# Optimization experiments

Measured on AMD Instinct MI355X. Metric: run time of the kernel, lower is better.

The kernel has to match this reference:

```python
import jax, jax.numpy as jnp
import numpy as np

TEMPERATURE = 0.1
EPS = 1e-8

# MatchingRuleAllViews defaults:
#   intra_view_same_class=1, intra_view_different_class=0,
#   inter_view_same_class=1, inter_view_different_class=0,
#   inter_image_same_class=-1, inter_image_different_class=-1,
#   self_similarity=-1

def setup_inputs() -> dict:
    key = jax.random.key(0)
    k1, k2, k3 = jax.random.split(key, 3)
    B, V, C, HW = 2, 2, 64, 1024
    student = jax.random.normal(k1, (B, V, C, HW), dtype=jnp.float32)
    teacher = jax.random.normal(k2, (B, V, C, HW), dtype=jnp.float32)
    labels = jax.random.randint(k3, (B, V, HW), 0, 5, dtype=jnp.int32)
    return {"student_embeddings": student, "teacher_embeddings": teacher, "labels": labels}


def _masks(B, V, HW, labels_flat):
    # image / view / pixel ids for each of the N = B*V*HW flattened positions
    image_ids = jnp.repeat(jnp.arange(B), V * HW)          # [N]
    view_ids = jnp.tile(jnp.repeat(jnp.arange(V), HW), B)  # [N]
    pixel_ids = jnp.tile(jnp.arange(HW), B * V)            # [N]
    si = image_ids[:, None] == image_ids[None, :]
    sv = view_ids[:, None] == view_ids[None, :]
    sp = pixel_ids[:, None] == pixel_ids[None, :]
    sc = labels_flat[:, None] == labels_flat[None, :]
    # default rule: same image -> (same class ? 1 : 0); different image -> -1;
    # self-similarity (same image, view, pixel) -> -1
    mask = jnp.where(si, jnp.where(sc, 1, 0), -1)
    mask = jnp.where(si & sv & sp, -1, mask)
    numerator_mask = (mask == 1).astype(jnp.float32)
    denom_mask = (mask >= 0).astype(jnp.float32)
    return numerator_mask, denom_mask


def reference(student_embeddings, teacher_embeddings, labels):
    B, V, C, HW = student_embeddings.shape
    N = B * V * HW
    # [B,V,C,HW] -> [N,C], L2-normalized
    sf = student_embeddings.transpose(0, 1, 3, 2).reshape(N, C)
    tf = teacher_embeddings.transpose(0, 1, 3, 2).reshape(N, C)
    sf = sf / jnp.linalg.norm(sf, axis=1, keepdims=True).clip(1e-12)
    tf = tf / jnp.linalg.norm(tf, axis=1, keepdims=True).clip(1e-12)
    logits = (sf @ tf.T) / TEMPERATURE  # [N,N]

    labels_flat = labels.reshape(-1)
    numerator_mask, denom_mask = _masks(B, V, HW, labels_flat)

    # masked log-softmax over dim 1 (denominator restricted to denom_mask)
    masked_logits = jnp.where(denom_mask > 0, logits, -jnp.inf)
    log_prob = jax.nn.log_softmax(masked_logits, axis=1)
    log_prob = jnp.where(jnp.isneginf(log_prob), 0.0, log_prob)

    numerator_sums = numerator_mask.sum(1)
    mean_log_prob_pos = (numerator_mask * log_prob).sum(1) / (numerator_sums + EPS)
    valid = numerator_sums > EPS  # [N] bool
    n_valid = valid.sum().astype(jnp.float32)
    loss = -jnp.sum(jnp.where(valid, mean_log_prob_pos, 0.0)) / n_valid

    # bg_anchors=False branch: (loss * non_bg[valid]).sum() / (non_bg[valid].sum() + eps)
    non_bg = (labels_flat != 0).astype(jnp.float32)
    non_bg_valid_sum = jnp.sum(non_bg * valid.astype(jnp.float32))
    loss = (loss * non_bg_valid_sum) / (non_bg_valid_sum + EPS)
    return loss
```

## Files before the change

### kernel.cpp

```cpp
#include <hip/hip_runtime.h>
#include <math.h>

#define NEG_INF (-1e30f)

typedef __attribute__((ext_vector_type(8))) short s16x8;
typedef __attribute__((ext_vector_type(4))) float f32x4;

__device__ __forceinline__ unsigned int pack_bf16(float lo, float hi) {
    unsigned int ul = __float_as_uint(lo);
    ul += 0x7FFFu + ((ul >> 16) & 1u);
    unsigned int uh = __float_as_uint(hi);
    uh += 0x7FFFu + ((uh >> 16) & 1u);
    return (ul >> 16) | (uh & 0xFFFF0000u);
}

__global__ __launch_bounds__(256, 2) void fused_scl_kernel(
    const float* __restrict__ s, const float* __restrict__ t,
    const int* __restrict__ labels, float4* __restrict__ stats,
    float* __restrict__ accums) {

    const int rb = blockIdx.x >> 4;
    const int jc = blockIdx.x & 15;
    const int img = rb >> 4;
    const int i0 = rb * 128;
    const int jb = img * 2048 + jc * 128;

    const int tid = threadIdx.x;

    __shared__ __align__(16) short lds_a[128 * 72];
    __shared__ __align__(16) short lds_b[128 * 72];
    __shared__ float lds_rs[128], lds_rt[128];
    __shared__ int lds_labi[128], lds_labj[128];

    if (blockIdx.x == 0 && tid < 8) accums[tid] = 0.f;

    if (tid < 128) lds_labi[tid] = labels[i0 + tid];
    else           lds_labj[tid - 128] = labels[jb + tid - 128];

    {
        const int t7 = tid & 7;
        const int pos4 = (tid >> 3) << 2;
        const int bvi = ((i0 >> 10) << 16) + (i0 & 1023) + pos4;
        const int bvj = ((jb >> 10) << 16) + (jb & 1023) + pos4;
        unsigned int* wa = (unsigned int*)lds_a;
        unsigned int* wb = (unsigned int*)lds_b;
#pragma unroll
        for (int k = 0; k < 4; ++k) {
            const int c0 = 2 * t7 + 16 * k;
            float4 a0 = *(const float4*)(s + bvi + c0 * 1024);
            float4 a1 = *(const float4*)(s + bvi + (c0 + 1) * 1024);
            float4 b0 = *(const float4*)(t + bvj + c0 * 1024);
            float4 b1 = *(const float4*)(t + bvj + (c0 + 1) * 1024);
            const int w = t7 + 8 * k;
            wa[36 * (pos4 + 0) + w] = pack_bf16(a0.x, a1.x);
            wa[36 * (pos4 + 1) + w] = pack_bf16(a0.y, a1.y);
            wa[36 * (pos4 + 2) + w] = pack_bf16(a0.z, a1.z);
            wa[36 * (pos4 + 3) + w] = pack_bf16(a0.w, a1.w);
            wb[36 * (pos4 + 0) + w] = pack_bf16(b0.x, b1.x);
            wb[36 * (pos4 + 1) + w] = pack_bf16(b0.y, b1.y);
            wb[36 * (pos4 + 2) + w] = pack_bf16(b0.z, b1.z);
            wb[36 * (pos4 + 3) + w] = pack_bf16(b0.w, b1.w);
        }
    }
    __syncthreads();

    {
        const int row = tid & 127;
        const unsigned int* wr =
            (const unsigned int*)((tid < 128) ? lds_a : lds_b) + 36 * row;
        float ssq = 0.f;
#pragma unroll
        for (int i = 0; i < 8; ++i) {
            uint4 u4 = *(const uint4*)(wr + 4 * i);
            const unsigned int uu[4] = {u4.x, u4.y, u4.z, u4.w};
#pragma unroll
            for (int q = 0; q < 4; ++q) {
                float lo = __uint_as_float(uu[q] << 16);
                float hi = __uint_as_float(uu[q] & 0xFFFF0000u);
                ssq = fmaf(lo, lo, ssq);
                ssq = fmaf(hi, hi, ssq);
            }
        }
        float r = 1.f / fmaxf(sqrtf(ssq), 1e-12f);
        if (tid < 128) lds_rs[row] = r;
        else           lds_rt[row] = r;
    }
    __syncthreads();

    const int lane = tid & 63;
    const int wv = tid >> 6;
    const int warow = wv << 5;
    const int quad = lane >> 4;
    const int col16 = lane & 15;

    s16x8 afr[2][2];
#pragma unroll
    for (int rt2 = 0; rt2 < 2; ++rt2) {
        const short* pa = lds_a + (warow + 16 * rt2 + col16) * 72 + 8 * quad;
        afr[rt2][0] = *(const s16x8*)pa;
        afr[rt2][1] = *(const s16x8*)(pa + 32);
    }

    f32x4 acc[2][8];
#pragma unroll
    for (int ct = 0; ct < 8; ++ct) {
        const short* pb = lds_b + (16 * ct + col16) * 72 + 8 * quad;
        s16x8 blo = *(const s16x8*)pb;
        s16x8 bhi = *(const s16x8*)(pb + 32);
#pragma unroll
        for (int rt2 = 0; rt2 < 2; ++rt2) {
            f32x4 z = {0.f, 0.f, 0.f, 0.f};
            z = __builtin_amdgcn_mfma_f32_16x16x32_bf16(afr[rt2][0], blo, z, 0, 0, 0);
            z = __builtin_amdgcn_mfma_f32_16x16x32_bf16(afr[rt2][1], bhi, z, 0, 0, 0);
            acc[rt2][ct] = z;
        }
    }

    float s_sum[8], A_sum[8], c_sum[8], rsi[8];
    int labi[8], ig[8];
#pragma unroll
    for (int rt2 = 0; rt2 < 2; ++rt2)
#pragma unroll
        for (int reg = 0; reg < 4; ++reg) {
            const int rr = rt2 * 4 + reg;
            const int rloc = warow + 16 * rt2 + 4 * quad + reg;
            rsi[rr] = lds_rs[rloc] * 10.f;
            labi[rr] = lds_labi[rloc];
            ig[rr] = i0 + rloc;
            s_sum[rr] = 0.f; A_sum[rr] = 0.f; c_sum[rr] = 0.f;
        }

#pragma unroll
    for (int ct = 0; ct < 8; ++ct) {
        const int jg = jb + 16 * ct + col16;
        const float rtj = lds_rt[16 * ct + col16];
        const int lj = lds_labj[16 * ct + col16];
#pragma unroll
        for (int rt2 = 0; rt2 < 2; ++rt2)
#pragma unroll
            for (int reg = 0; reg < 4; ++reg) {
                const int rr = rt2 * 4 + reg;
                float logit = acc[rt2][ct][reg] * rsi[rr] * rtj;
                bool self = (jg == ig[rr]);
                float e = __expf((self ? NEG_INF : logit) - 10.f);
                s_sum[rr] += e;
                if (!self && lj == labi[rr]) { A_sum[rr] += logit; c_sum[rr] += 1.f; }
            }
    }

#pragma unroll
    for (int off = 1; off < 16; off <<= 1)
#pragma unroll
        for (int rr = 0; rr < 8; ++rr) {
            s_sum[rr] += __shfl_xor(s_sum[rr], off, 64);
            A_sum[rr] += __shfl_xor(A_sum[rr], off, 64);
            c_sum[rr] += __shfl_xor(c_sum[rr], off, 64);
        }

    if (col16 == 0) {
#pragma unroll
        for (int rr = 0; rr < 8; ++rr)
            stats[ig[rr] * 16 + jc] =
                make_float4(s_sum[rr], A_sum[rr], c_sum[rr], 0.f);
    }
}

__global__ __launch_bounds__(256) void finalize_kernel(
    const float4* __restrict__ stats, const int* __restrict__ labels,
    float* __restrict__ accums, float* __restrict__ out) {
    const int tid = threadIdx.x;
    const int r = blockIdx.x * 256 + tid;

    float ssum = 0.f, A = 0.f, cnt = 0.f;
#pragma unroll
    for (int c = 0; c < 16; ++c) {
        float4 v = stats[r * 16 + c];
        ssum += v.x; A += v.y; cnt += v.z;
    }
    float mlpp = 0.f, val = 0.f, nbv = 0.f;
    if (cnt > 0.5f) {
        float lse = 10.f + __logf(ssum);
        mlpp = (A - cnt * lse) / (cnt + 1e-8f);
        val = 1.f;
        nbv = (labels[r] != 0) ? 1.f : 0.f;
    }

    __shared__ float red0[256], red1[256], red2[256];
    red0[tid] = mlpp; red1[tid] = val; red2[tid] = nbv;
    __syncthreads();
    for (int off = 128; off > 0; off >>= 1) {
        if (tid < off) {
            red0[tid] += red0[tid + off];
            red1[tid] += red1[tid + off];
            red2[tid] += red2[tid + off];
        }
        __syncthreads();
    }

    if (tid == 0) {
        atomicAdd(&accums[0], red0[0]);
        atomicAdd(&accums[1], red1[0]);
        atomicAdd(&accums[2], red2[0]);
        __threadfence();
        unsigned int old = atomicAdd((unsigned int*)&accums[3], 1u);
        if (old == 15u) {
            float S = atomicAdd(&accums[0], 0.f);
            float V = atomicAdd(&accums[1], 0.f);
            float NB = atomicAdd(&accums[2], 0.f);
            float loss = -S / V;
            out[0] = loss * NB / (NB + 1e-8f);
        }
    }
}

extern "C" void kernel_launch(void* const* d_in, const int* in_sizes, int n_in,
                              void* d_out, int out_size, void* d_ws, size_t ws_size,
                              hipStream_t stream) {
    const float* s = (const float*)d_in[0];
    const float* t = (const float*)d_in[1];
    const int* labels = (const int*)d_in[2];
    float* out = (float*)d_out;

    float* accums = (float*)d_ws;
    float4* stats = (float4*)((char*)d_ws + 32);

    hipLaunchKernelGGL(fused_scl_kernel, dim3(512), dim3(256), 0, stream,
                       s, t, labels, stats, accums);
    hipLaunchKernelGGL(finalize_kernel, dim3(16), dim3(256), 0, stream,
                       stats, labels, accums, out);
}
```

Measured before the change: 74.21 us.

## Split normalization and bf16 packing into a prep kernel feeding LDS-free GEMM

Adds a prep kernel that L2-normalizes student and teacher rows once and writes them as bf16 in a row-major workspace layout. The main kernel then loads MFMA fragments straight from global memory with no LDS staging or barriers, and the per-element rescaling by inverse norms goes away. Before, each block re-read and re-converted its fp32 tiles, so every tile was loaded 16 times. The cost is an extra kernel launch and a workspace round trip. Normalizing before rounding to bf16 also changes the numerics slightly.

```diff
diff --git a/kernel.cpp b/kernel.cpp
--- a/kernel.cpp
+++ b/kernel.cpp
@@ -14,10 +14,81 @@
     return (ul >> 16) | (uh & 0xFFFF0000u);
 }
 
-__global__ __launch_bounds__(256, 2) void fused_scl_kernel(
+__global__ __launch_bounds__(256) void prep_kernel(
     const float* __restrict__ s, const float* __restrict__ t,
-    const int* __restrict__ labels, float4* __restrict__ stats,
+    unsigned int* __restrict__ sbf, unsigned int* __restrict__ tbf,
     float* __restrict__ accums) {
+    const int b = blockIdx.x;
+    const int tid = threadIdx.x;
+    const int n0 = (b & 63) << 6;
+    const float* __restrict__ src = (b >= 64) ? t : s;
+    unsigned int* __restrict__ dst = (b >= 64) ? tbf : sbf;
+
+    if (b == 0 && tid < 8) accums[tid] = 0.f;
+
+    __shared__ __align__(16) float lds[64][68];
+    __shared__ float red[4][64];
+    __shared__ float rinv[64];
+
+    {
+        const int cg = tid & 15;
+        const int pos4 = (tid >> 4) << 2;
+        const int base = ((n0 >> 10) << 16) + (n0 & 1023) + pos4;
+#pragma unroll
+        for (int cc = 0; cc < 4; ++cc) {
+            const int c = (cg << 2) + cc;
+            float4 v = *(const float4*)(src + base + (c << 10));
+            lds[pos4 + 0][c] = v.x;
+            lds[pos4 + 1][c] = v.y;
+            lds[pos4 + 2][c] = v.z;
+            lds[pos4 + 3][c] = v.w;
+        }
+    }
+    __syncthreads();
+
+    {
+        const int pos = tid & 63;
+        const int q = tid >> 6;
+        float ssq = 0.f;
+#pragma unroll
+        for (int j = 0; j < 4; ++j) {
+            float4 v = *(const float4*)&lds[pos][(q << 4) + (j << 2)];
+            ssq = fmaf(v.x, v.x, ssq);
+            ssq = fmaf(v.y, v.y, ssq);
+            ssq = fmaf(v.z, v.z, ssq);
+            ssq = fmaf(v.w, v.w, ssq);
+        }
+        red[q][pos] = ssq;
+    }
+    __syncthreads();
+    if (tid < 64) {
+        float v = red[0][tid] + red[1][tid] + red[2][tid] + red[3][tid];
+        rinv[tid] = 1.f / fmaxf(sqrtf(v), 1e-12f);
+    }
+    __syncthreads();
+
+    {
+        const int pos = tid >> 2;
+        const int o0 = (tid & 3) << 1;
+        const float r = rinv[pos];
+        unsigned int* drow = dst + ((n0 + pos) << 5);
+#pragma unroll
+        for (int oo = 0; oo < 2; ++oo) {
+            const int o = o0 + oo;
+            const float* lp = &lds[pos][o << 3];
+            uint4 u;
+            u.x = pack_bf16(lp[0] * r, lp[1] * r);
+            u.y = pack_bf16(lp[2] * r, lp[3] * r);
+            u.z = pack_bf16(lp[4] * r, lp[5] * r);
+            u.w = pack_bf16(lp[6] * r, lp[7] * r);
+            *(uint4*)(drow + (o << 2)) = u;
+        }
+    }
+}
+
+__global__ __launch_bounds__(256, 2) void main_kernel(
+    const s16x8* __restrict__ sbf, const s16x8* __restrict__ tbf,
+    const int* __restrict__ labels, float4* __restrict__ stats) {
 
     const int rb = blockIdx.x >> 4;
     const int jc = blockIdx.x & 15;
@@ -26,67 +97,6 @@
     const int jb = img * 2048 + jc * 128;
 
     const int tid = threadIdx.x;
-
-    __shared__ __align__(16) short lds_a[128 * 72];
-    __shared__ __align__(16) short lds_b[128 * 72];
-    __shared__ float lds_rs[128], lds_rt[128];
-    __shared__ int lds_labi[128], lds_labj[128];
-
-    if (blockIdx.x == 0 && tid < 8) accums[tid] = 0.f;
-
-    if (tid < 128) lds_labi[tid] = labels[i0 + tid];
-    else           lds_labj[tid - 128] = labels[jb + tid - 128];
-
-    {
-        const int t7 = tid & 7;
-        const int pos4 = (tid >> 3) << 2;
-        const int bvi = ((i0 >> 10) << 16) + (i0 & 1023) + pos4;
-        const int bvj = ((jb >> 10) << 16) + (jb & 1023) + pos4;
-        unsigned int* wa = (unsigned int*)lds_a;
-        unsigned int* wb = (unsigned int*)lds_b;
-#pragma unroll
-        for (int k = 0; k < 4; ++k) {
-            const int c0 = 2 * t7 + 16 * k;
-            float4 a0 = *(const float4*)(s + bvi + c0 * 1024);
-            float4 a1 = *(const float4*)(s + bvi + (c0 + 1) * 1024);
-            float4 b0 = *(const float4*)(t + bvj + c0 * 1024);
-            float4 b1 = *(const float4*)(t + bvj + (c0 + 1) * 1024);
-            const int w = t7 + 8 * k;
-            wa[36 * (pos4 + 0) + w] = pack_bf16(a0.x, a1.x);
-            wa[36 * (pos4 + 1) + w] = pack_bf16(a0.y, a1.y);
-            wa[36 * (pos4 + 2) + w] = pack_bf16(a0.z, a1.z);
-            wa[36 * (pos4 + 3) + w] = pack_bf16(a0.w, a1.w);
-            wb[36 * (pos4 + 0) + w] = pack_bf16(b0.x, b1.x);
-            wb[36 * (pos4 + 1) + w] = pack_bf16(b0.y, b1.y);
-            wb[36 * (pos4 + 2) + w] = pack_bf16(b0.z, b1.z);
-            wb[36 * (pos4 + 3) + w] = pack_bf16(b0.w, b1.w);
-        }
-    }
-    __syncthreads();
-
-    {
-        const int row = tid & 127;
-        const unsigned int* wr =
-            (const unsigned int*)((tid < 128) ? lds_a : lds_b) + 36 * row;
-        float ssq = 0.f;
-#pragma unroll
-        for (int i = 0; i < 8; ++i) {
-            uint4 u4 = *(const uint4*)(wr + 4 * i);
-            const unsigned int uu[4] = {u4.x, u4.y, u4.z, u4.w};
-#pragma unroll
-            for (int q = 0; q < 4; ++q) {
-                float lo = __uint_as_float(uu[q] << 16);
-                float hi = __uint_as_float(uu[q] & 0xFFFF0000u);
-                ssq = fmaf(lo, lo, ssq);
-                ssq = fmaf(hi, hi, ssq);
-            }
-        }
-        float r = 1.f / fmaxf(sqrtf(ssq), 1e-12f);
-        if (tid < 128) lds_rs[row] = r;
-        else           lds_rt[row] = r;
-    }
-    __syncthreads();
-
     const int lane = tid & 63;
     const int wv = tid >> 6;
     const int warow = wv << 5;
@@ -95,57 +105,56 @@
 
     s16x8 afr[2][2];
 #pragma unroll
-    for (int rt2 = 0; rt2 < 2; ++rt2) {
-        const short* pa = lds_a + (warow + 16 * rt2 + col16) * 72 + 8 * quad;
-        afr[rt2][0] = *(const s16x8*)pa;
-        afr[rt2][1] = *(const s16x8*)(pa + 32);
-    }
-
-    f32x4 acc[2][8];
+    for (int rt = 0; rt < 2; ++rt) {
+        const int row = i0 + warow + 16 * rt + col16;
+#pragma unroll
+        for (int kh = 0; kh < 2; ++kh)
+            afr[rt][kh] = sbf[row * 8 + quad + 4 * kh];
+    }
+    s16x8 bfr[8][2];
 #pragma unroll
     for (int ct = 0; ct < 8; ++ct) {
-        const short* pb = lds_b + (16 * ct + col16) * 72 + 8 * quad;
-        s16x8 blo = *(const s16x8*)pb;
-        s16x8 bhi = *(const s16x8*)(pb + 32);
-#pragma unroll
-        for (int rt2 = 0; rt2 < 2; ++rt2) {
-            f32x4 z = {0.f, 0.f, 0.f, 0.f};
-            z = __builtin_amdgcn_mfma_f32_16x16x32_bf16(afr[rt2][0], blo, z, 0, 0, 0);
-            z = __builtin_amdgcn_mfma_f32_16x16x32_bf16(afr[rt2][1], bhi, z, 0, 0, 0);
-            acc[rt2][ct] = z;
-        }
-    }
-
-    float s_sum[8], A_sum[8], c_sum[8], rsi[8];
+        const int col = jb + 16 * ct + col16;
+#pragma unroll
+        for (int kh = 0; kh < 2; ++kh)
+            bfr[ct][kh] = tbf[col * 8 + quad + 4 * kh];
+    }
+
     int labi[8], ig[8];
 #pragma unroll
-    for (int rt2 = 0; rt2 < 2; ++rt2)
+    for (int rt = 0; rt < 2; ++rt)
 #pragma unroll
         for (int reg = 0; reg < 4; ++reg) {
-            const int rr = rt2 * 4 + reg;
-            const int rloc = warow + 16 * rt2 + 4 * quad + reg;
-            rsi[rr] = lds_rs[rloc] * 10.f;
-            labi[rr] = lds_labi[rloc];
-            ig[rr] = i0 + rloc;
-            s_sum[rr] = 0.f; A_sum[rr] = 0.f; c_sum[rr] = 0.f;
-        }
+            const int rr = rt * 4 + reg;
+            ig[rr] = i0 + warow + 16 * rt + 4 * quad + reg;
+            labi[rr] = labels[ig[rr]];
+        }
+    int lj[8];
+#pragma unroll
+    for (int ct = 0; ct < 8; ++ct) lj[ct] = labels[jb + 16 * ct + col16];
+
+    float s_sum[8], A_sum[8], c_sum[8];
+#pragma unroll
+    for (int rr = 0; rr < 8; ++rr) { s_sum[rr] = 0.f; A_sum[rr] = 0.f; c_sum[rr] = 0.f; }
 
 #pragma unroll
     for (int ct = 0; ct < 8; ++ct) {
         const int jg = jb + 16 * ct + col16;
-        const float rtj = lds_rt[16 * ct + col16];
-        const int lj = lds_labj[16 * ct + col16];
-#pragma unroll
-        for (int rt2 = 0; rt2 < 2; ++rt2)
+#pragma unroll
+        for (int rt = 0; rt < 2; ++rt) {
+            f32x4 z = {0.f, 0.f, 0.f, 0.f};
+            z = __builtin_amdgcn_mfma_f32_16x16x32_bf16(afr[rt][0], bfr[ct][0], z, 0, 0, 0);
+            z = __builtin_amdgcn_mfma_f32_16x16x32_bf16(afr[rt][1], bfr[ct][1], z, 0, 0, 0);
 #pragma unroll
             for (int reg = 0; reg < 4; ++reg) {
-                const int rr = rt2 * 4 + reg;
-                float logit = acc[rt2][ct][reg] * rsi[rr] * rtj;
+                const int rr = rt * 4 + reg;
+                float logit = z[reg] * 10.f;
                 bool self = (jg == ig[rr]);
                 float e = __expf((self ? NEG_INF : logit) - 10.f);
                 s_sum[rr] += e;
-                if (!self && lj == labi[rr]) { A_sum[rr] += logit; c_sum[rr] += 1.f; }
+                if (!self && lj[ct] == labi[rr]) { A_sum[rr] += logit; c_sum[rr] += 1.f; }
             }
+        }
     }
 
 #pragma unroll
@@ -160,8 +169,7 @@
     if (col16 == 0) {
 #pragma unroll
         for (int rr = 0; rr < 8; ++rr)
-            stats[ig[rr] * 16 + jc] =
-                make_float4(s_sum[rr], A_sum[rr], c_sum[rr], 0.f);
+            stats[ig[rr] * 16 + jc] = make_float4(s_sum[rr], A_sum[rr], c_sum[rr], 0.f);
     }
 }
 
@@ -221,11 +229,16 @@
     const int* labels = (const int*)d_in[2];
     float* out = (float*)d_out;
 
-    float* accums = (float*)d_ws;
-    float4* stats = (float4*)((char*)d_ws + 32);
-
-    hipLaunchKernelGGL(fused_scl_kernel, dim3(512), dim3(256), 0, stream,
-                       s, t, labels, stats, accums);
+    char* ws = (char*)d_ws;
+    float* accums = (float*)ws;
+    unsigned int* sbf = (unsigned int*)(ws + 1024);
+    unsigned int* tbf = (unsigned int*)(ws + 1024 + 524288);
+    float4* stats = (float4*)(ws + 1024 + 2 * 524288);
+
+    hipLaunchKernelGGL(prep_kernel, dim3(128), dim3(256), 0, stream,
+                       s, t, sbf, tbf, accums);
+    hipLaunchKernelGGL(main_kernel, dim3(512), dim3(256), 0, stream,
+                       (const s16x8*)sbf, (const s16x8*)tbf, labels, stats);
     hipLaunchKernelGGL(finalize_kernel, dim3(16), dim3(256), 0, stream,
                        stats, labels, accums, out);
 }
```

Result: slower. 76.59 us (+3.2%).
